# Performance work log

Hardware: AMD Instinct MI355X
Metric: run time of the kernel (lower is better)

The kernel has to match this reference:

```python
import jax, jax.numpy as jnp
import numpy as np

EPS = 1e-4  # IRLS smoothing epsilon

def _corr(x, k):
    # x: [C,H,W], k: [kh,kw]; cross-correlation, 'same' output, replicate (clamp) boundary
    ph, pw = k.shape[0] // 2, k.shape[1] // 2
    xp = jnp.pad(x, ((0, 0), (ph, ph), (pw, pw)), mode='edge')
    out = jax.lax.conv_general_dilated(xp[:, None], k[None, None].astype(x.dtype), (1, 1), 'VALID', dimension_numbers=('NCHW', 'OIHW', 'NCHW'))
    return out[:, 0]

def _flip(k):
    return k[::-1, ::-1]

def _forward(blurred, kernel, reg_kernels, reg_kernel_weights, reg_target_kernels, reg_powers, num_irls_iter, num_cg_iter):
    n = reg_kernels.shape[0]
    w_kernel = jnp.ones_like(blurred)                       # data-term weights (ones, as in forward)
    w_reg = jnp.ones((n,) + blurred.shape, blurred.dtype)   # IRLS reg weights, start at 1
    lam = reg_kernel_weights ** 2                           # squared weights keep A PSD

    def R(x, ks):  # apply each reg kernel -> [N,C,H,W]
        return jax.vmap(lambda k: _corr(x, k))(ks)

    def RT(y, ks):  # adjoint: correlate with flipped kernels, y: [N,C,H,W]
        return jax.vmap(lambda yi, k: _corr(yi, _flip(k)))(y, ks)

    def A(x, w_reg):  # A = K^T W K + sum_n lam_n R_n^T W_n R_n
        data = _corr(w_kernel * _corr(x, kernel), _flip(kernel))
        reg = jnp.einsum('n,nchw->chw', lam, RT(w_reg * R(x, reg_kernels), reg_kernels))
        return data + reg

    Tb = R(blurred, reg_target_kernels)           # regularization targets T_n b
    KtWb = _corr(w_kernel * blurred, _flip(kernel))
    x0 = blurred
    for _ in range(num_irls_iter):
        # DeconvCGInit: rhs and initial residual/search direction
        rhs = KtWb + jnp.einsum('n,nchw->chw', lam, RT(w_reg * Tb, reg_kernels))
        x = x0
        r = rhs - A(x, w_reg)
        p = r
        # DeconvCGIter: standard CG updates
        for _ in range(num_cg_iter):
            Ap = A(p, w_reg)
            rr = jnp.sum(r * r)
            alpha = rr / jnp.sum(p * Ap)
            x = x + alpha * p
            r = r - alpha * Ap
            beta = jnp.sum(r * r) / rr
            p = r + beta * p
        x0 = x
        # DeconvCGWeight: IRLS reweighting w_n = p_n * (|R_n x - T_n b| + eps)^(p_n - 2)
        d = R(x0, reg_kernels) - Tb
        pw = reg_powers[:, None, None, None]
        w_reg = pw * jnp.power(jnp.abs(d) + EPS, pw - 2.0)
    return x0

def setup_inputs():
    key = jax.random.key(0)
    ks = jax.random.split(key, 6)
    C, H, W = 3, 1024, 1024
    NREG, RKS, BKS = 5, 5, 15
    blurred = jax.random.uniform(ks[0], (C, H, W), jnp.float32)
    kernel = jax.random.uniform(ks[1], (BKS, BKS), jnp.float32)
    kernel = kernel / jnp.sum(kernel)  # normalized blur kernel
    rk = 0.1 * jax.random.normal(ks[2], (NREG, RKS, RKS), jnp.float32)
    rk = rk.at[0, 2, 2].add(-2.0).at[0, 3, 2].add(1.0).at[0, 2, 3].add(1.0)  # gradient stencil init
    rkw = 0.1 * jax.random.normal(ks[3], (NREG,), jnp.float32)
    rkw = rkw.at[0].add(1.0)
    rtk = 0.1 * jax.random.normal(ks[4], (NREG, RKS, RKS), jnp.float32)
    rp = 1.0 + 0.02 * jax.random.normal(ks[5], (NREG,), jnp.float32)
    return {"blurred": blurred, "kernel": kernel, "reg_kernels": rk, "reg_kernel_weights": rkw, "reg_target_kernels": rtk, "reg_powers": rp, "num_irls_iter": 2, "num_cg_iter": 4}

def reference(blurred, kernel, reg_kernels, reg_kernel_weights, reg_target_kernels, reg_powers, num_irls_iter, num_cg_iter):
    return _forward(blurred, kernel, reg_kernels, reg_kernel_weights, reg_target_kernels, reg_powers, num_irls_iter, num_cg_iter)
```

## Files before the change

### kernel.cpp

```cpp
#include <hip/hip_runtime.h>
#include <math.h>

#define HH 1024
#define WW 1024
#define CHN 3
#define PLANE (HH*WW)
#define IMG (CHN*PLANE)
#define NREG 5
#define EPSV 1e-4f

#define OFF_WREG 0
#define OFF_KTWB (5*IMG)
#define OFF_T    (6*IMG)
#define OFF_R    (7*IMG)
#define OFF_P    (8*IMG)
#define OFF_AP   (9*IMG)
#define OFF_PART (10*IMG)

__global__ __launch_bounds__(256) void k_init(const float4* __restrict__ b,
                                              float4* __restrict__ x,
                                              float4* __restrict__ wreg) {
  const int stride = gridDim.x * 256;
  const float4 one = make_float4(1.f, 1.f, 1.f, 1.f);
  for (int i = blockIdx.x * 256 + threadIdx.x; i < NREG * IMG / 4; i += stride) {
    wreg[i] = one;
    if (i < IMG / 4) x[i] = b[i];
  }
}

template <bool FLIP>
__global__ __launch_bounds__(128) void k_corr15(const float* __restrict__ in,
                                                const float* __restrict__ k15,
                                                float* __restrict__ out) {
  __shared__ float tile[78 * 87];
  __shared__ float kpad[15 * 16];
  const int ch = blockIdx.z;
  const int R0 = blockIdx.y * 64;
  const int C0 = blockIdx.x * 72;
  const int tid = threadIdx.x;
  for (int i = tid; i < 240; i += 128) {
    int a = i >> 4, b = i & 15;
    float v = 0.f;
    if (b < 15) v = FLIP ? k15[(14 - a) * 15 + (14 - b)] : k15[a * 15 + b];
    kpad[i] = v;
  }
  const float* inc = in + ch * PLANE;
  for (int i = tid; i < 78 * 86; i += 128) {
    int r = i / 86, c = i - r * 86;
    int gr = min(max(R0 - 7 + r, 0), HH - 1);
    int gc = min(max(C0 - 7 + c, 0), WW - 1);
    tile[r * 87 + c] = inc[gr * WW + gc];
  }
  __syncthreads();
  const int tx = tid & 7, ty = tid >> 3;
  const int oi = ty * 4, oj = tx * 9;
  float acc[4][9];
#pragma unroll
  for (int o = 0; o < 4; ++o)
#pragma unroll
    for (int q = 0; q < 9; ++q) acc[o][q] = 0.f;

#pragma unroll 1
  for (int rr = 0; rr < 18; ++rr) {
    float wv[23];
#pragma unroll
    for (int q = 0; q < 23; ++q) wv[q] = tile[(oi + rr) * 87 + oj + q];
#pragma unroll
    for (int o = 0; o < 4; ++o) {
      int a = rr - o;
      if ((unsigned)a < 15u) {
        const float4* kp = (const float4*)&kpad[a * 16];
        float4 kA = kp[0], kB = kp[1], kC = kp[2], kD = kp[3];
        float kv[16] = {kA.x, kA.y, kA.z, kA.w, kB.x, kB.y, kB.z, kB.w,
                        kC.x, kC.y, kC.z, kC.w, kD.x, kD.y, kD.z, kD.w};
#pragma unroll
        for (int b = 0; b < 15; ++b)
#pragma unroll
          for (int q = 0; q < 9; ++q)
            acc[o][q] = fmaf(kv[b], wv[b + q], acc[o][q]);
      }
    }
  }
  float* oc = out + ch * PLANE;
#pragma unroll
  for (int o = 0; o < 4; ++o) {
    const int orow = R0 + oi + o;
#pragma unroll
    for (int q = 0; q < 9; ++q) {
      int gcol = C0 + oj + q;
      if (gcol < WW) oc[orow * WW + gcol] = acc[o][q];
    }
  }
}

__device__ __forceinline__ void blk_reduce2(float a, float b, float* scratch,
                                            float* o1, float* o2) {
#pragma unroll
  for (int off = 32; off > 0; off >>= 1) {
    a += __shfl_down(a, off, 64);
    b += __shfl_down(b, off, 64);
  }
  __syncthreads();
  const int lane = threadIdx.x & 63, wid = threadIdx.x >> 6;
  if (lane == 0) { scratch[wid] = a; scratch[4 + wid] = b; }
  __syncthreads();
  if (threadIdx.x == 0) {
    *o1 = scratch[0] + scratch[1] + scratch[2] + scratch[3];
    *o2 = scratch[4] + scratch[5] + scratch[6] + scratch[7];
  }
}

template <int MODE>
__global__ __launch_bounds__(256) void k_reg(
    const float* __restrict__ src, const float* __restrict__ kin_all,
    const float* __restrict__ rk, const float* __restrict__ rkw,
    const float* __restrict__ wreg, const float* __restrict__ ktwb,
    float* __restrict__ ap, const float* __restrict__ rin,
    float* __restrict__ rout, float* __restrict__ pout,
    float* __restrict__ part) {
  __shared__ float sbuf[72 * 73];
  __shared__ float vbuf[68 * 69];
  __shared__ float kin_s[NREG * 25];
  __shared__ float kf_s[NREG * 25];
  __shared__ float scratch[8];
  const int ch = blockIdx.z;
  const int R0 = blockIdx.y * 64, C0 = blockIdx.x * 64;
  const int tid = threadIdx.x;
  const int lane = tid & 63, wid = tid >> 6;
  const int W = wid * 16;

  if (tid < NREG * 25) {
    int n = tid / 25, j = tid - n * 25, a = j / 5, b = j - a * 5;
    kin_s[tid] = kin_all[tid];
    float lw = rkw[n];
    kf_s[tid] = lw * lw * rk[n * 25 + (4 - a) * 5 + (4 - b)];
  }
  const float* sc = src + ch * PLANE;
  for (int i = tid; i < 72 * 72; i += 256) {
    int r = i / 72, c = i - r * 72;
    int gr = min(max(R0 - 4 + r, 0), HH - 1);
    int gc = min(max(C0 - 4 + c, 0), WW - 1);
    sbuf[r * 73 + c] = sc[gr * WW + gc];
  }
  __syncthreads();

  float acc[16];
#pragma unroll
  for (int s = 0; s < 16; ++s) acc[s] = 0.f;

  for (int n = 0; n < NREG; ++n) {
    float kin[25];
#pragma unroll
    for (int j = 0; j < 25; ++j) kin[j] = kin_s[n * 25 + j];
    const float* wn = wreg + (n * CHN + ch) * PLANE;

    for (int e = tid; e < 528; e += 256) {
      int vr, vc;
      if (e < 136)      { vr = e / 68;                 vc = e - (e / 68) * 68; }
      else if (e < 272) { int j2 = e - 136; vr = 66 + j2 / 68; vc = j2 - (j2 / 68) * 68; }
      else if (e < 400) { int j2 = e - 272; vr = 2 + (j2 >> 1); vc = j2 & 1; }
      else              { int j2 = e - 400; vr = 2 + (j2 >> 1); vc = 66 + (j2 & 1); }
      int rc = min(max(R0 - 2 + vr, 0), HH - 1);
      int cc = min(max(C0 - 2 + vc, 0), WW - 1);
      int tr = rc - R0 + 2, tc = cc - C0 + 2;
      float s = 0.f;
#pragma unroll
      for (int a = 0; a < 5; ++a)
#pragma unroll
        for (int b = 0; b < 5; ++b)
          s = fmaf(kin[a * 5 + b], sbuf[(tr + a) * 73 + tc + b], s);
      vbuf[vr * 69 + vc] = s * wn[rc * WW + cc];
    }

    float vacc[16];
#pragma unroll
    for (int s = 0; s < 16; ++s) vacc[s] = 0.f;
#pragma unroll
    for (int rr = 0; rr < 20; ++rr) {
      float x5[5];
#pragma unroll
      for (int b = 0; b < 5; ++b) x5[b] = sbuf[(W + 2 + rr) * 73 + lane + 2 + b];
#pragma unroll
      for (int a = 0; a < 5; ++a) {
        int s = rr - a;
        if (s >= 0 && s < 16) {
#pragma unroll
          for (int b = 0; b < 5; ++b) vacc[s] = fmaf(kin[a * 5 + b], x5[b], vacc[s]);
        }
      }
    }
#pragma unroll
    for (int s = 0; s < 16; ++s)
      vbuf[(2 + W + s) * 69 + lane + 2] = vacc[s] * wn[(R0 + W + s) * WW + C0 + lane];
    __syncthreads();

    float kf[25];
#pragma unroll
    for (int j = 0; j < 25; ++j) kf[j] = kf_s[n * 25 + j];
#pragma unroll
    for (int rv = 0; rv < 20; ++rv) {
      float v5[5];
#pragma unroll
      for (int b = 0; b < 5; ++b) v5[b] = vbuf[(W + rv) * 69 + lane + b];
#pragma unroll
      for (int a = 0; a < 5; ++a) {
        int s = rv - a;
        if (s >= 0 && s < 16) {
#pragma unroll
          for (int b = 0; b < 5; ++b) acc[s] = fmaf(kf[a * 5 + b], v5[b], acc[s]);
        }
      }
    }
    __syncthreads();
  }

  const int obase = ch * PLANE + (R0 + W) * WW + C0 + lane;
  if constexpr (MODE == 2) {
#pragma unroll
    for (int s = 0; s < 16; ++s) {
      float rv = ktwb[obase + s * WW] - ap[obase + s * WW] + acc[s];
      rout[obase + s * WW] = rv;
      pout[obase + s * WW] = rv;
    }
  } else {
    float pap = 0.f, rr2 = 0.f;
#pragma unroll
    for (int s = 0; s < 16; ++s) {
      float av = ap[obase + s * WW] + acc[s];
      ap[obase + s * WW] = av;
      if constexpr (MODE == 0) {
        float pv = src[obase + s * WW];
        float rv = rin[obase + s * WW];
        pap = fmaf(av, pv, pap);
        rr2 = fmaf(rv, rv, rr2);
      }
    }
    if constexpr (MODE == 0) {
      float s1, s2;
      blk_reduce2(pap, rr2, scratch, &s1, &s2);
      if (tid == 0) {
        int bid = (blockIdx.z * 16 + blockIdx.y) * 16 + blockIdx.x;
        part[bid] = s1;
        part[1024 + bid] = s2;
      }
    }
  }
}

__global__ __launch_bounds__(256) void k_wupd(
    const float* __restrict__ x, const float* __restrict__ blur,
    const float* __restrict__ rk, const float* __restrict__ rtk,
    const float* __restrict__ rp, float* __restrict__ wreg) {
  __shared__ float xb[68 * 69];
  __shared__ float bb[68 * 69];
  __shared__ float k1s[NREG * 25], k2s[NREG * 25];
  __shared__ float rps[NREG];
  const int ch = blockIdx.z, R0 = blockIdx.y * 64, C0 = blockIdx.x * 64;
  const int tid = threadIdx.x;
  const int lane = tid & 63, wid = tid >> 6, W = wid * 16;
  if (tid < NREG * 25) { k1s[tid] = rk[tid]; k2s[tid] = rtk[tid]; }
  if (tid < NREG) rps[tid] = rp[tid];
  const float* xc = x + ch * PLANE;
  const float* bc = blur + ch * PLANE;
  for (int i = tid; i < 68 * 68; i += 256) {
    int r = i / 68, c = i - r * 68;
    int gr = min(max(R0 - 2 + r, 0), HH - 1);
    int gc = min(max(C0 - 2 + c, 0), WW - 1);
    xb[r * 69 + c] = xc[gr * WW + gc];
    bb[r * 69 + c] = bc[gr * WW + gc];
  }
  __syncthreads();
  for (int n = 0; n < NREG; ++n) {
    float k1[25], k2[25];
#pragma unroll
    for (int j = 0; j < 25; ++j) { k1[j] = k1s[n * 25 + j]; k2[j] = k2s[n * 25 + j]; }
    float d_[16];
#pragma unroll
    for (int s = 0; s < 16; ++s) d_[s] = 0.f;
#pragma unroll
    for (int rr = 0; rr < 20; ++rr) {
      float x5[5], b5[5];
#pragma unroll
      for (int b = 0; b < 5; ++b) {
        x5[b] = xb[(W + rr) * 69 + lane + b];
        b5[b] = bb[(W + rr) * 69 + lane + b];
      }
#pragma unroll
      for (int a = 0; a < 5; ++a) {
        int s = rr - a;
        if (s >= 0 && s < 16) {
#pragma unroll
          for (int b = 0; b < 5; ++b) {
            d_[s] = fmaf(k1[a * 5 + b], x5[b], d_[s]);
            d_[s] = fmaf(-k2[a * 5 + b], b5[b], d_[s]);
          }
        }
      }
    }
    float pw = rps[n];
    float* wc = wreg + (n * CHN + ch) * PLANE + (R0 + W) * WW + C0 + lane;
#pragma unroll
    for (int s = 0; s < 16; ++s) {
      float v = fabsf(d_[s]) + EPSV;
      wc[s * WW] = pw * __expf((pw - 2.f) * __logf(v));
    }
  }
}

__global__ __launch_bounds__(256) void k_upd_xr(
    float4* __restrict__ x, const float4* __restrict__ p,
    float4* __restrict__ r, const float4* __restrict__ ap,
    const float* __restrict__ part, float* __restrict__ part2) {
  __shared__ float scratch[8];
  __shared__ float sAlpha;
  {
    float a = 0.f, b = 0.f;
    for (int i = threadIdx.x; i < 768; i += 256) {
      a += part[i];
      b += part[1024 + i];
    }
    float s1, s2;
    blk_reduce2(a, b, scratch, &s1, &s2);
    if (threadIdx.x == 0) sAlpha = s2 / s1;
    __syncthreads();
  }
  const float alpha = sAlpha;
  float s = 0.f;
  const int stride = gridDim.x * 256;
  for (int i = blockIdx.x * 256 + threadIdx.x; i < IMG / 4; i += stride) {
    float4 xv = x[i], pv = p[i], rv = r[i], av = ap[i];
    xv.x += alpha * pv.x; xv.y += alpha * pv.y; xv.z += alpha * pv.z; xv.w += alpha * pv.w;
    rv.x -= alpha * av.x; rv.y -= alpha * av.y; rv.z -= alpha * av.z; rv.w -= alpha * av.w;
    x[i] = xv; r[i] = rv;
    s += rv.x * rv.x + rv.y * rv.y + rv.z * rv.z + rv.w * rv.w;
  }
#pragma unroll
  for (int off = 32; off > 0; off >>= 1) s += __shfl_down(s, off, 64);
  __syncthreads();
  if ((threadIdx.x & 63) == 0) scratch[threadIdx.x >> 6] = s;
  __syncthreads();
  if (threadIdx.x == 0)
    part2[blockIdx.x] = scratch[0] + scratch[1] + scratch[2] + scratch[3];
}

__global__ __launch_bounds__(256) void k_upd_x(
    float4* __restrict__ x, const float4* __restrict__ p,
    const float* __restrict__ part) {
  __shared__ float scratch[8];
  __shared__ float sAlpha;
  {
    float a = 0.f, b = 0.f;
    for (int i = threadIdx.x; i < 768; i += 256) {
      a += part[i];
      b += part[1024 + i];
    }
    float s1, s2;
    blk_reduce2(a, b, scratch, &s1, &s2);
    if (threadIdx.x == 0) sAlpha = s2 / s1;
    __syncthreads();
  }
  const float alpha = sAlpha;
  const int stride = gridDim.x * 256;
  for (int i = blockIdx.x * 256 + threadIdx.x; i < IMG / 4; i += stride) {
    float4 xv = x[i], pv = p[i];
    xv.x += alpha * pv.x; xv.y += alpha * pv.y; xv.z += alpha * pv.z; xv.w += alpha * pv.w;
    x[i] = xv;
  }
}

__global__ __launch_bounds__(256) void k_upd_p(
    float4* __restrict__ p, const float4* __restrict__ r,
    const float* __restrict__ part, const float* __restrict__ part2) {
  __shared__ float scratch[8];
  __shared__ float sBeta;
  {
    float a = 0.f, b = 0.f;
    for (int i = threadIdx.x; i < 768; i += 256) {
      a += part2[i];
      b += part[1024 + i];
    }
    float s1, s2;
    blk_reduce2(a, b, scratch, &s1, &s2);
    if (threadIdx.x == 0) sBeta = s1 / s2;
    __syncthreads();
  }
  const float beta = sBeta;
  const int stride = gridDim.x * 256;
  for (int i = blockIdx.x * 256 + threadIdx.x; i < IMG / 4; i += stride) {
    float4 pv = p[i], rv = r[i];
    pv.x = rv.x + beta * pv.x; pv.y = rv.y + beta * pv.y;
    pv.z = rv.z + beta * pv.z; pv.w = rv.w + beta * pv.w;
    p[i] = pv;
  }
}

extern "C" void kernel_launch(void* const* d_in, const int* in_sizes, int n_in,
                              void* d_out, int out_size, void* d_ws, size_t ws_size,
                              hipStream_t stream) {
  (void)in_sizes; (void)n_in; (void)out_size; (void)ws_size;
  const float* blurred = (const float*)d_in[0];
  const float* k15 = (const float*)d_in[1];
  const float* rk  = (const float*)d_in[2];
  const float* rkw = (const float*)d_in[3];
  const float* rtk = (const float*)d_in[4];
  const float* rp  = (const float*)d_in[5];

  float* x = (float*)d_out;
  float* ws = (float*)d_ws;
  float* wreg  = ws + OFF_WREG;
  float* ktwb  = ws + OFF_KTWB;
  float* t     = ws + OFF_T;
  float* r     = ws + OFF_R;
  float* p     = ws + OFF_P;
  float* ap    = ws + OFF_AP;
  float* part  = ws + OFF_PART;
  float* part2 = part + 2048;

  const dim3 b256(256), b128(128);
  const dim3 g15(15, 16, CHN);
  const dim3 g64(16, 16, CHN);

  k_init<<<dim3(2048), b256, 0, stream>>>((const float4*)blurred, (float4*)x,
                                          (float4*)wreg);
  k_corr15<true><<<g15, b128, 0, stream>>>(blurred, k15, ktwb);

  for (int irls = 0; irls < 2; ++irls) {
    k_corr15<false><<<g15, b128, 0, stream>>>(x, k15, t);
    k_corr15<true><<<g15, b128, 0, stream>>>(t, k15, ap);
    k_reg<1><<<g64, b256, 0, stream>>>(x, rk, rk, rkw, wreg, nullptr, ap,
                                       nullptr, nullptr, nullptr, nullptr);
    k_reg<2><<<g64, b256, 0, stream>>>(blurred, rtk, rk, rkw, wreg, ktwb, ap,
                                       nullptr, r, p, nullptr);
    for (int cg = 0; cg < 4; ++cg) {
      const bool last = (cg == 3);
      k_corr15<false><<<g15, b128, 0, stream>>>(p, k15, t);
      k_corr15<true><<<g15, b128, 0, stream>>>(t, k15, ap);
      k_reg<0><<<g64, b256, 0, stream>>>(p, rk, rk, rkw, wreg, nullptr, ap,
                                         r, nullptr, nullptr, part);
      if (!last) {
        k_upd_xr<<<dim3(768), b256, 0, stream>>>((float4*)x, (const float4*)p,
                                                 (float4*)r, (const float4*)ap,
                                                 part, part2);
        k_upd_p<<<dim3(768), b256, 0, stream>>>((float4*)p, (const float4*)r,
                                                part, part2);
      } else {
        k_upd_x<<<dim3(768), b256, 0, stream>>>((float4*)x, (const float4*)p, part);
      }
    }
    if (irls == 0)
      k_wupd<<<g64, b256, 0, stream>>>(x, blurred, rk, rtk, rp, wreg);
  }
}
```

Before: 1.654 ms.

## Skip unit reg weights in first IRLS pass and retile conv kernels

Drops the 5-image initialization of IRLS weights to one and adds a W1 template path that skips reading the weights while they are still all ones in the first IRLS iteration. The 15x15 correlation kernel moves to 256 threads with 2 output rows per thread, and the regularization kernel uses 32-row tiles. The partial-sum buffers and reductions grow to match the doubled block count. This removes the memory traffic of writing and reading weights that are known to be one, and raises parallelism, at the cost of more halo recomputation per output.

```diff
diff --git a/kernel.cpp b/kernel.cpp
--- a/kernel.cpp
+++ b/kernel.cpp
@@ -18,18 +18,14 @@
 #define OFF_PART (10*IMG)
 
 __global__ __launch_bounds__(256) void k_init(const float4* __restrict__ b,
-                                              float4* __restrict__ x,
-                                              float4* __restrict__ wreg) {
+                                              float4* __restrict__ x) {
   const int stride = gridDim.x * 256;
-  const float4 one = make_float4(1.f, 1.f, 1.f, 1.f);
-  for (int i = blockIdx.x * 256 + threadIdx.x; i < NREG * IMG / 4; i += stride) {
-    wreg[i] = one;
-    if (i < IMG / 4) x[i] = b[i];
-  }
+  for (int i = blockIdx.x * 256 + threadIdx.x; i < IMG / 4; i += stride)
+    x[i] = b[i];
 }
 
 template <bool FLIP>
-__global__ __launch_bounds__(128) void k_corr15(const float* __restrict__ in,
+__global__ __launch_bounds__(256) void k_corr15(const float* __restrict__ in,
                                                 const float* __restrict__ k15,
                                                 float* __restrict__ out) {
   __shared__ float tile[78 * 87];
@@ -38,14 +34,14 @@
   const int R0 = blockIdx.y * 64;
   const int C0 = blockIdx.x * 72;
   const int tid = threadIdx.x;
-  for (int i = tid; i < 240; i += 128) {
-    int a = i >> 4, b = i & 15;
+  if (tid < 240) {
+    int a = tid >> 4, b = tid & 15;
     float v = 0.f;
     if (b < 15) v = FLIP ? k15[(14 - a) * 15 + (14 - b)] : k15[a * 15 + b];
-    kpad[i] = v;
+    kpad[tid] = v;
   }
   const float* inc = in + ch * PLANE;
-  for (int i = tid; i < 78 * 86; i += 128) {
+  for (int i = tid; i < 78 * 86; i += 256) {
     int r = i / 86, c = i - r * 86;
     int gr = min(max(R0 - 7 + r, 0), HH - 1);
     int gc = min(max(C0 - 7 + c, 0), WW - 1);
@@ -53,20 +49,20 @@
   }
   __syncthreads();
   const int tx = tid & 7, ty = tid >> 3;
-  const int oi = ty * 4, oj = tx * 9;
-  float acc[4][9];
-#pragma unroll
-  for (int o = 0; o < 4; ++o)
+  const int oi = ty * 2, oj = tx * 9;
+  float acc[2][9];
+#pragma unroll
+  for (int o = 0; o < 2; ++o)
 #pragma unroll
     for (int q = 0; q < 9; ++q) acc[o][q] = 0.f;
 
 #pragma unroll 1
-  for (int rr = 0; rr < 18; ++rr) {
+  for (int rr = 0; rr < 16; ++rr) {
     float wv[23];
 #pragma unroll
     for (int q = 0; q < 23; ++q) wv[q] = tile[(oi + rr) * 87 + oj + q];
 #pragma unroll
-    for (int o = 0; o < 4; ++o) {
+    for (int o = 0; o < 2; ++o) {
       int a = rr - o;
       if ((unsigned)a < 15u) {
         const float4* kp = (const float4*)&kpad[a * 16];
@@ -83,7 +79,7 @@
   }
   float* oc = out + ch * PLANE;
 #pragma unroll
-  for (int o = 0; o < 4; ++o) {
+  for (int o = 0; o < 2; ++o) {
     const int orow = R0 + oi + o;
 #pragma unroll
     for (int q = 0; q < 9; ++q) {
@@ -110,7 +106,7 @@
   }
 }
 
-template <int MODE>
+template <int MODE, bool W1>
 __global__ __launch_bounds__(256) void k_reg(
     const float* __restrict__ src, const float* __restrict__ kin_all,
     const float* __restrict__ rk, const float* __restrict__ rkw,
@@ -118,16 +114,16 @@
     float* __restrict__ ap, const float* __restrict__ rin,
     float* __restrict__ rout, float* __restrict__ pout,
     float* __restrict__ part) {
-  __shared__ float sbuf[72 * 73];
-  __shared__ float vbuf[68 * 69];
+  __shared__ float sbuf[40 * 73];
+  __shared__ float vbuf[36 * 69];
   __shared__ float kin_s[NREG * 25];
   __shared__ float kf_s[NREG * 25];
   __shared__ float scratch[8];
   const int ch = blockIdx.z;
-  const int R0 = blockIdx.y * 64, C0 = blockIdx.x * 64;
+  const int R0 = blockIdx.y * 32, C0 = blockIdx.x * 64;
   const int tid = threadIdx.x;
   const int lane = tid & 63, wid = tid >> 6;
-  const int W = wid * 16;
+  const int W = wid * 8;
 
   if (tid < NREG * 25) {
     int n = tid / 25, j = tid - n * 25, a = j / 5, b = j - a * 5;
@@ -136,7 +132,7 @@
     kf_s[tid] = lw * lw * rk[n * 25 + (4 - a) * 5 + (4 - b)];
   }
   const float* sc = src + ch * PLANE;
-  for (int i = tid; i < 72 * 72; i += 256) {
+  for (int i = tid; i < 40 * 72; i += 256) {
     int r = i / 72, c = i - r * 72;
     int gr = min(max(R0 - 4 + r, 0), HH - 1);
     int gc = min(max(C0 - 4 + c, 0), WW - 1);
@@ -144,9 +140,9 @@
   }
   __syncthreads();
 
-  float acc[16];
-#pragma unroll
-  for (int s = 0; s < 16; ++s) acc[s] = 0.f;
+  float acc[8];
+#pragma unroll
+  for (int s = 0; s < 8; ++s) acc[s] = 0.f;
 
   for (int n = 0; n < NREG; ++n) {
     float kin[25];
@@ -154,58 +150,64 @@
     for (int j = 0; j < 25; ++j) kin[j] = kin_s[n * 25 + j];
     const float* wn = wreg + (n * CHN + ch) * PLANE;
 
-    for (int e = tid; e < 528; e += 256) {
+    for (int e = tid; e < 400; e += 256) {
       int vr, vc;
-      if (e < 136)      { vr = e / 68;                 vc = e - (e / 68) * 68; }
-      else if (e < 272) { int j2 = e - 136; vr = 66 + j2 / 68; vc = j2 - (j2 / 68) * 68; }
-      else if (e < 400) { int j2 = e - 272; vr = 2 + (j2 >> 1); vc = j2 & 1; }
-      else              { int j2 = e - 400; vr = 2 + (j2 >> 1); vc = 66 + (j2 & 1); }
+      if (e < 136)      { vr = e / 68;            vc = e - (e / 68) * 68; }
+      else if (e < 272) { int j2 = e - 136; vr = 34 + j2 / 68; vc = j2 - (j2 / 68) * 68; }
+      else              { int j2 = e - 272; vr = 2 + (j2 >> 2);
+                          int m = j2 & 3; vc = (m < 2) ? m : 64 + m; }
       int rc = min(max(R0 - 2 + vr, 0), HH - 1);
       int cc = min(max(C0 - 2 + vc, 0), WW - 1);
-      int tr = rc - R0 + 2, tc = cc - C0 + 2;
+      int tr = rc - R0 + 4, tc = cc - C0 + 4;
       float s = 0.f;
 #pragma unroll
       for (int a = 0; a < 5; ++a)
 #pragma unroll
         for (int b = 0; b < 5; ++b)
-          s = fmaf(kin[a * 5 + b], sbuf[(tr + a) * 73 + tc + b], s);
-      vbuf[vr * 69 + vc] = s * wn[rc * WW + cc];
-    }
-
-    float vacc[16];
-#pragma unroll
-    for (int s = 0; s < 16; ++s) vacc[s] = 0.f;
-#pragma unroll
-    for (int rr = 0; rr < 20; ++rr) {
+          s = fmaf(kin[a * 5 + b], sbuf[(tr - 2 + a) * 73 + tc - 2 + b], s);
+      vbuf[vr * 69 + vc] = W1 ? s : s * wn[rc * WW + cc];
+    }
+
+    float vacc[8];
+#pragma unroll
+    for (int s = 0; s < 8; ++s) vacc[s] = 0.f;
+#pragma unroll
+    for (int rr = 0; rr < 12; ++rr) {
       float x5[5];
 #pragma unroll
-      for (int b = 0; b < 5; ++b) x5[b] = sbuf[(W + 2 + rr) * 73 + lane + 2 + b];
+      for (int b = 0; b < 5; ++b) x5[b] = sbuf[(2 + W + rr) * 73 + lane + 2 + b];
 #pragma unroll
       for (int a = 0; a < 5; ++a) {
         int s = rr - a;
-        if (s >= 0 && s < 16) {
+        if (s >= 0 && s < 8) {
 #pragma unroll
           for (int b = 0; b < 5; ++b) vacc[s] = fmaf(kin[a * 5 + b], x5[b], vacc[s]);
         }
       }
     }
-#pragma unroll
-    for (int s = 0; s < 16; ++s)
-      vbuf[(2 + W + s) * 69 + lane + 2] = vacc[s] * wn[(R0 + W + s) * WW + C0 + lane];
+    if constexpr (W1) {
+#pragma unroll
+      for (int s = 0; s < 8; ++s)
+        vbuf[(2 + W + s) * 69 + lane + 2] = vacc[s];
+    } else {
+#pragma unroll
+      for (int s = 0; s < 8; ++s)
+        vbuf[(2 + W + s) * 69 + lane + 2] = vacc[s] * wn[(R0 + W + s) * WW + C0 + lane];
+    }
     __syncthreads();
 
     float kf[25];
 #pragma unroll
     for (int j = 0; j < 25; ++j) kf[j] = kf_s[n * 25 + j];
 #pragma unroll
-    for (int rv = 0; rv < 20; ++rv) {
+    for (int rv = 0; rv < 12; ++rv) {
       float v5[5];
 #pragma unroll
       for (int b = 0; b < 5; ++b) v5[b] = vbuf[(W + rv) * 69 + lane + b];
 #pragma unroll
       for (int a = 0; a < 5; ++a) {
         int s = rv - a;
-        if (s >= 0 && s < 16) {
+        if (s >= 0 && s < 8) {
 #pragma unroll
           for (int b = 0; b < 5; ++b) acc[s] = fmaf(kf[a * 5 + b], v5[b], acc[s]);
         }
@@ -217,7 +219,7 @@
   const int obase = ch * PLANE + (R0 + W) * WW + C0 + lane;
   if constexpr (MODE == 2) {
 #pragma unroll
-    for (int s = 0; s < 16; ++s) {
+    for (int s = 0; s < 8; ++s) {
       float rv = ktwb[obase + s * WW] - ap[obase + s * WW] + acc[s];
       rout[obase + s * WW] = rv;
       pout[obase + s * WW] = rv;
@@ -225,7 +227,7 @@
   } else {
     float pap = 0.f, rr2 = 0.f;
 #pragma unroll
-    for (int s = 0; s < 16; ++s) {
+    for (int s = 0; s < 8; ++s) {
       float av = ap[obase + s * WW] + acc[s];
       ap[obase + s * WW] = av;
       if constexpr (MODE == 0) {
@@ -239,9 +241,9 @@
       float s1, s2;
       blk_reduce2(pap, rr2, scratch, &s1, &s2);
       if (tid == 0) {
-        int bid = (blockIdx.z * 16 + blockIdx.y) * 16 + blockIdx.x;
+        int bid = (blockIdx.z * 32 + blockIdx.y) * 16 + blockIdx.x;
         part[bid] = s1;
-        part[1024 + bid] = s2;
+        part[2048 + bid] = s2;
       }
     }
   }
@@ -315,9 +317,9 @@
   __shared__ float sAlpha;
   {
     float a = 0.f, b = 0.f;
-    for (int i = threadIdx.x; i < 768; i += 256) {
+    for (int i = threadIdx.x; i < 1536; i += 256) {
       a += part[i];
-      b += part[1024 + i];
+      b += part[2048 + i];
     }
     float s1, s2;
     blk_reduce2(a, b, scratch, &s1, &s2);
@@ -350,9 +352,9 @@
   __shared__ float sAlpha;
   {
     float a = 0.f, b = 0.f;
-    for (int i = threadIdx.x; i < 768; i += 256) {
+    for (int i = threadIdx.x; i < 1536; i += 256) {
       a += part[i];
-      b += part[1024 + i];
+      b += part[2048 + i];
     }
     float s1, s2;
     blk_reduce2(a, b, scratch, &s1, &s2);
@@ -375,9 +377,9 @@
   __shared__ float sBeta;
   {
     float a = 0.f, b = 0.f;
-    for (int i = threadIdx.x; i < 768; i += 256) {
-      a += part2[i];
-      b += part[1024 + i];
+    for (int i = threadIdx.x; i < 1536; i += 256) {
+      if (i < 768) a += part2[i];
+      b += part[2048 + i];
     }
     float s1, s2;
     blk_reduce2(a, b, scratch, &s1, &s2);
@@ -414,29 +416,40 @@
   float* p     = ws + OFF_P;
   float* ap    = ws + OFF_AP;
   float* part  = ws + OFF_PART;
-  float* part2 = part + 2048;
-
-  const dim3 b256(256), b128(128);
+  float* part2 = part + 4096;
+
+  const dim3 b256(256);
   const dim3 g15(15, 16, CHN);
+  const dim3 gRG(16, 32, CHN);
   const dim3 g64(16, 16, CHN);
 
-  k_init<<<dim3(2048), b256, 0, stream>>>((const float4*)blurred, (float4*)x,
-                                          (float4*)wreg);
-  k_corr15<true><<<g15, b128, 0, stream>>>(blurred, k15, ktwb);
+  k_init<<<dim3(768), b256, 0, stream>>>((const float4*)blurred, (float4*)x);
+  k_corr15<true><<<g15, b256, 0, stream>>>(blurred, k15, ktwb);
 
   for (int irls = 0; irls < 2; ++irls) {
-    k_corr15<false><<<g15, b128, 0, stream>>>(x, k15, t);
-    k_corr15<true><<<g15, b128, 0, stream>>>(t, k15, ap);
-    k_reg<1><<<g64, b256, 0, stream>>>(x, rk, rk, rkw, wreg, nullptr, ap,
-                                       nullptr, nullptr, nullptr, nullptr);
-    k_reg<2><<<g64, b256, 0, stream>>>(blurred, rtk, rk, rkw, wreg, ktwb, ap,
-                                       nullptr, r, p, nullptr);
+    k_corr15<false><<<g15, b256, 0, stream>>>(x, k15, t);
+    k_corr15<true><<<g15, b256, 0, stream>>>(t, k15, ap);
+    if (irls == 0) {
+      k_reg<1, true><<<gRG, b256, 0, stream>>>(x, rk, rk, rkw, wreg, nullptr, ap,
+                                               nullptr, nullptr, nullptr, nullptr);
+      k_reg<2, true><<<gRG, b256, 0, stream>>>(blurred, rtk, rk, rkw, wreg, ktwb, ap,
+                                               nullptr, r, p, nullptr);
+    } else {
+      k_reg<1, false><<<gRG, b256, 0, stream>>>(x, rk, rk, rkw, wreg, nullptr, ap,
+                                                nullptr, nullptr, nullptr, nullptr);
+      k_reg<2, false><<<gRG, b256, 0, stream>>>(blurred, rtk, rk, rkw, wreg, ktwb, ap,
+                                                nullptr, r, p, nullptr);
+    }
     for (int cg = 0; cg < 4; ++cg) {
       const bool last = (cg == 3);
-      k_corr15<false><<<g15, b128, 0, stream>>>(p, k15, t);
-      k_corr15<true><<<g15, b128, 0, stream>>>(t, k15, ap);
-      k_reg<0><<<g64, b256, 0, stream>>>(p, rk, rk, rkw, wreg, nullptr, ap,
-                                         r, nullptr, nullptr, part);
+      k_corr15<false><<<g15, b256, 0, stream>>>(p, k15, t);
+      k_corr15<true><<<g15, b256, 0, stream>>>(t, k15, ap);
+      if (irls == 0)
+        k_reg<0, true><<<gRG, b256, 0, stream>>>(p, rk, rk, rkw, wreg, nullptr, ap,
+                                                 r, nullptr, nullptr, part);
+      else
+        k_reg<0, false><<<gRG, b256, 0, stream>>>(p, rk, rk, rkw, wreg, nullptr, ap,
+                                                  r, nullptr, nullptr, part);
       if (!last) {
         k_upd_xr<<<dim3(768), b256, 0, stream>>>((float4*)x, (const float4*)p,
                                                  (float4*)r, (const float4*)ap,
```

New measurement: 1.567 ms. 1.06x faster.
